# Kernel optimization log

Hardware: AMD Instinct MI355X
Metric: run time of the kernel (lower is better)

The kernel has to match this reference:

```python
import jax, jax.numpy as jnp
import numpy as np

MAX_NORM = 1.0 - 1e-5


def _norm(x):
    return jnp.sqrt(jnp.sum(x * x, axis=-1, keepdims=True) + 1e-15)


def project(x):
    n = _norm(x)
    return jnp.where(n > MAX_NORM, x * (MAX_NORM / n), x)


def artanh(x):
    return jnp.arctanh(jnp.clip(x, -1.0 + 1e-7, 1.0 - 1e-7))


def expmap0(u):
    n = _norm(u)
    return project(jnp.tanh(n) * u / n)


def logmap0(x):
    x = project(x)
    n = _norm(x)
    return artanh(n) * x / n


def mobius_add(x, y):
    x2 = jnp.sum(x * x, -1, keepdims=True)
    y2 = jnp.sum(y * y, -1, keepdims=True)
    xy = jnp.sum(x * y, -1, keepdims=True)
    num = (1.0 + 2.0 * xy + y2) * x + (1.0 - x2) * y
    den = 1.0 + 2.0 * xy + x2 * y2
    return project(num / den)


def mobius_matvec(M, x):
    # M: [d, d]; x: [..., d]  ->  expmap0(M @ logmap0(x))
    return expmap0(jnp.einsum('...d,ed->...e', logmap0(x), M))


def mobius_pw(w, x):
    # pointwise (diagonal) mobius scaling
    return expmap0(w * logmap0(x))


def hyper_gru(seq, Wz, Wr, Wh, Uz, Ur, Uh, bz, br, bh):
    # seq: [S, B, H, d] -> outputs [S, B, H, d]; state is H points per sample in a d-dim Poincare ball
    def cell(h, x):
        z = jax.nn.sigmoid(logmap0(mobius_add(mobius_add(mobius_matvec(Wz, h), mobius_matvec(Uz, x)), bz)))
        r = jax.nn.sigmoid(logmap0(mobius_add(mobius_add(mobius_matvec(Wr, h), mobius_matvec(Ur, x)), br)))
        h_tilde = mobius_add(mobius_add(mobius_matvec(Wh, mobius_pw(r, h)), mobius_matvec(Uh, x)), bh)
        h_new = mobius_add(h, mobius_pw(z, mobius_add(-h, h_tilde)))
        return h_new, h_new
    h0 = jnp.zeros_like(seq[0])
    _, outs = jax.lax.scan(cell, h0, seq)
    return outs


def poinc_dist_sum(enc, lab):
    # enc: [B,S,H,d] (in-ball), lab: [L,H,d] (in-ball) -> sum_H poinc_dist : [B,S,L]
    e2 = jnp.sum(enc * enc, -1)                      # [B,S,H]
    l2 = jnp.sum(lab * lab, -1)                      # [L,H]
    el = jnp.einsum('bshd,lhd->bslh', enc, lab)      # [B,S,L,H] (avoids [B,S,L,H,d] diff)
    d2 = e2[:, :, None, :] + l2[None, None, :, :] - 2.0 * el
    denom = (1.0 - e2)[:, :, None, :] * (1.0 - l2)[None, None, :, :]
    z = 1.0 + 2.0 * d2 / jnp.maximum(denom, 1e-15)
    dist = jnp.arccosh(jnp.maximum(z, 1.0 + 1e-7))
    return jnp.sum(dist, axis=-1)                    # [B,S,L]


def _forward(x, word_embed, label_embed, Wz, Wr, Wh, Uz, Ur, Uh, bz, br, bh, W1, b1, W2, b2):
    we = project(word_embed)[x]                      # [B,S,H,d]
    seq = jnp.transpose(we, (1, 0, 2, 3))            # [S,B,H,d]
    outs = hyper_gru(seq, Wz, Wr, Wh, Uz, Ur, Uh, bz, br, bh)
    enc = jnp.transpose(outs, (0, 1, 2, 3))
    enc = jnp.transpose(outs, (1, 0, 2, 3))          # [B,S,H,d]
    inter = poinc_dist_sum(enc, project(label_embed))  # [B,S,L]
    inter = jnp.transpose(inter, (0, 2, 1))          # [B,L,S]
    h = jax.nn.relu(inter @ W1.T + b1)               # [B,L,S//2]
    out = (h @ W2.T + b2)[..., 0]                    # [B,L]
    return out


def setup_inputs() -> dict:
    key = jax.random.key(0)
    ks = jax.random.split(key, 16)
    B, S, L, H, D, V = 4, 512, 512, 32, 8, 30000
    sc = 1.0 / np.sqrt(D)
    x = jax.random.randint(ks[0], (B, S), 0, V)
    inp = {
        'x': x,
        'word_embed': 0.05 * jax.random.normal(ks[1], (V, H, D), jnp.float32),
        'label_embed': 0.05 * jax.random.normal(ks[2], (L, H, D), jnp.float32),
        'Wz': sc * jax.random.normal(ks[3], (D, D), jnp.float32),
        'Wr': sc * jax.random.normal(ks[4], (D, D), jnp.float32),
        'Wh': sc * jax.random.normal(ks[5], (D, D), jnp.float32),
        'Uz': sc * jax.random.normal(ks[6], (D, D), jnp.float32),
        'Ur': sc * jax.random.normal(ks[7], (D, D), jnp.float32),
        'Uh': sc * jax.random.normal(ks[8], (D, D), jnp.float32),
        'bz': 0.01 * jax.random.normal(ks[9], (D,), jnp.float32),
        'br': 0.01 * jax.random.normal(ks[10], (D,), jnp.float32),
        'bh': 0.01 * jax.random.normal(ks[11], (D,), jnp.float32),
        'W1': jax.random.normal(ks[12], (S // 2, S), jnp.float32) / np.sqrt(S),
        'b1': jnp.zeros((S // 2,), jnp.float32),
        'W2': jax.random.normal(ks[13], (1, S // 2), jnp.float32) / np.sqrt(S // 2),
        'b2': jnp.zeros((1,), jnp.float32),
    }
    return inp


def reference(x, word_embed, label_embed, Wz, Wr, Wh, Uz, Ur, Uh, bz, br, bh, W1, b1, W2, b2):
    return _forward(x, word_embed, label_embed, Wz, Wr, Wh, Uz, Ur, Uh, bz, br, bh, W1, b1, W2, b2)
```

## Files before the change

kernel.cpp:

```cpp
#include <hip/hip_runtime.h>
#include <math.h>

#define DEV __device__ __forceinline__

static constexpr int BB = 4, SS = 512, LL = 512, HH = 32;
static constexpr float MAXN  = 1.0f - 1e-5f;
static constexpr float MAXN2 = MAXN * MAXN;

DEV float rcpf(float x) { return __builtin_amdgcn_rcpf(x); }
DEV float rsqf(float x) { return __builtin_amdgcn_rsqf(x); }

DEV float dot8(const float* a, const float* b) {
  float s0 = a[0]*b[0], s1 = a[1]*b[1], s2 = a[2]*b[2], s3 = a[3]*b[3];
  float s4 = a[4]*b[4], s5 = a[5]*b[5], s6 = a[6]*b[6], s7 = a[7]*b[7];
  return ((s0+s1)+(s2+s3)) + ((s4+s5)+(s6+s7));
}

DEV void load8(float* d, const float* p) {
  float4 a = *(const float4*)p;
  float4 b = *(const float4*)(p + 4);
  d[0]=a.x; d[1]=a.y; d[2]=a.z; d[3]=a.w;
  d[4]=b.x; d[5]=b.y; d[6]=b.z; d[7]=b.w;
}

DEV void store8(float* p, const float* d) {
  *(float4*)p       = make_float4(d[0], d[1], d[2], d[3]);
  *(float4*)(p + 4) = make_float4(d[4], d[5], d[6], d[7]);
}

DEV void project8(float* x) {
  float n2 = dot8(x, x) + 1e-15f;
  if (n2 > MAXN2) {
    float s = MAXN * rsqf(n2);
    #pragma unroll
    for (int i = 0; i < 8; ++i) x[i] *= s;
  }
}

DEV void logmap0_8(float* o, const float* x) {
  float t[8];
  #pragma unroll
  for (int i = 0; i < 8; ++i) t[i] = x[i];
  project8(t);
  float n2 = dot8(t, t) + 1e-15f;
  float rs = rsqf(n2);
  float n  = n2 * rs;
  float c  = fminf(n, 1.0f - 1e-7f);
  float at = 0.34657359f * (__log2f(1.0f + c) - __log2f(1.0f - c));
  float r  = at * rs;
  #pragma unroll
  for (int i = 0; i < 8; ++i) o[i] = t[i] * r;
}

DEV void expmap0_8(float* o, const float* u) {
  float n2 = dot8(u, u) + 1e-15f;
  float rs = rsqf(n2);
  float n  = n2 * rs;
  float e  = __expf(2.0f * n);
  float th = 1.0f - 2.0f * rcpf(e + 1.0f);
  float r  = th * rs;
  #pragma unroll
  for (int i = 0; i < 8; ++i) o[i] = u[i] * r;
  project8(o);
}

DEV void matvec8(float* o, const float* M, const float* u) {
  #pragma unroll
  for (int e = 0; e < 8; ++e) o[e] = dot8(M + 8*e, u);
}

template<int CTRL>
DEV float dppf(float x) {
  int xi = __float_as_int(x);
  return __int_as_float(__builtin_amdgcn_update_dpp(xi, xi, CTRL, 0xF, 0xF, true));
}

DEV float grp8sum(float x) {
  x += dppf<0xB1>(x);
  x += dppf<0x4E>(x);
  x += dppf<0x141>(x);
  return x;
}

DEV void red2(float& a, float& b) {
  float t0 = dppf<0xB1>(a),  t1 = dppf<0xB1>(b);  a += t0; b += t1;
  float t2 = dppf<0x4E>(a),  t3 = dppf<0x4E>(b);  a += t2; b += t3;
  float t4 = dppf<0x141>(a), t5 = dppf<0x141>(b); a += t4; b += t5;
}

DEV void red3(float& a, float& b, float& c) {
  float t0 = dppf<0xB1>(a),  t1 = dppf<0xB1>(b),  t2 = dppf<0xB1>(c);
  a += t0; b += t1; c += t2;
  float t3 = dppf<0x4E>(a),  t4 = dppf<0x4E>(b),  t5 = dppf<0x4E>(c);
  a += t3; b += t4; c += t5;
  float t6 = dppf<0x141>(a), t7 = dppf<0x141>(b), t8 = dppf<0x141>(c);
  a += t6; b += t7; c += t8;
}

DEV void red4(float& a, float& b, float& c, float& d) {
  float t0 = dppf<0xB1>(a),  t1 = dppf<0xB1>(b),  t2 = dppf<0xB1>(c),  t3 = dppf<0xB1>(d);
  a += t0; b += t1; c += t2; d += t3;
  float t4 = dppf<0x4E>(a),  t5 = dppf<0x4E>(b),  t6 = dppf<0x4E>(c),  t7 = dppf<0x4E>(d);
  a += t4; b += t5; c += t6; d += t7;
  float t8 = dppf<0x141>(a), t9 = dppf<0x141>(b), ta = dppf<0x141>(c), tb = dppf<0x141>(d);
  a += t8; b += t9; c += ta; d += tb;
}

#define MV8(w, u0,u1,u2,u3,u4,u5,u6,u7) \
  ((((w[0]*(u0)) + (w[1]*(u1))) + ((w[2]*(u2)) + (w[3]*(u3)))) + \
   (((w[4]*(u4)) + (w[5]*(u5))) + ((w[6]*(u6)) + (w[7]*(u7)))))

DEV float lgscale(float n2) {
  float n2p = n2 + 1e-15f;
  float rs  = rsqf(n2p);
  float n   = n2p * rs;
  float c   = fminf(n, 1.0f - 1e-7f);
  float at  = 0.34657359f * (__log2f(1.0f + c) - __log2f(1.0f - c));
  return at * rs;
}

DEV float sigm(float x) { return rcpf(1.0f + __expf(-x)); }

DEV void gate_coeffs(float n2v, float dvc, float dvb,
                     float c2, float b2, float cb,
                     float& P, float& Q, float& R, float& g2_2) {
  float n2p = n2v + 1e-15f;
  float rsv = rsqf(n2p);
  float nv  = n2p * rsv;
  float e   = __expf(2.0f * nv);
  float th  = 1.0f - 2.0f * rcpf(e + 1.0f);
  float a_scale = th * rsv;
  float a2  = th * th;
  if (a2 > MAXN2) { float s = MAXN * rsqf(a2); a_scale *= s; a2 = MAXN2; }
  float xy1 = a_scale * dvc;
  float cx1 = 1.0f + 2.0f*xy1 + c2;
  float cy1 = 1.0f - a2;
  float rd1 = rcpf(1.0f + 2.0f*xy1 + a2*c2);
  float num2 = (cx1*cx1)*a2 + 2.0f*(cx1*cy1)*xy1 + (cy1*cy1)*c2;
  float g1_2 = num2 * (rd1*rd1);
  float e1 = rd1;
  if (g1_2 > MAXN2) { e1 *= MAXN * rsqf(g1_2); g1_2 = MAXN2; }
  float ab  = a_scale * dvb;
  float xy2 = e1 * (cx1*ab + cy1*cb);
  float cx2 = 1.0f + 2.0f*xy2 + b2;
  float cy2 = 1.0f - g1_2;
  float rd2 = rcpf(1.0f + 2.0f*xy2 + g1_2*b2);
  float n2b = (cx2*cx2)*g1_2 + 2.0f*(cx2*cy2)*xy2 + (cy2*cy2)*b2;
  g2_2 = n2b * (rd2*rd2);
  float e2s = rd2;
  if (g2_2 > MAXN2) { e2s *= MAXN * rsqf(g2_2); g2_2 = MAXN2; }
  float t = e2s * cx2 * e1;
  P = t * cx1 * a_scale;
  Q = t * cy1;
  R = e2s * cy2;
}

__global__ void prep_kernel(const int* __restrict__ x, const float* __restrict__ wemb,
                            const float* __restrict__ Uz, const float* __restrict__ Ur,
                            const float* __restrict__ Uh,
                            const float* __restrict__ bzp, const float* __restrict__ brp,
                            const float* __restrict__ bhp,
                            float* __restrict__ axz, float* __restrict__ axr, float* __restrict__ axh,
                            float* __restrict__ scB)
{
  int t = blockIdx.x * 256 + threadIdx.x;
  if (t >= BB * SS * HH) return;
  int hh = t & (HH - 1);
  int bs = t >> 5;
  int idx = x[bs];
  float we[8]; load8(we, wemb + ((size_t)idx * HH + hh) * 8);
  project8(we);
  float lx[8]; logmap0_8(lx, we);
  float bz[8], br[8], bh[8];
  load8(bz, bzp); load8(br, brp); load8(bh, bhp);
  float v[8], az[8], ar[8], ah[8];
  matvec8(v, Uz, lx); expmap0_8(az, v); store8(axz + (size_t)t * 8, az);
  matvec8(v, Ur, lx); expmap0_8(ar, v); store8(axr + (size_t)t * 8, ar);
  matvec8(v, Uh, lx); expmap0_8(ah, v); store8(axh + (size_t)t * 8, ah);
  float cz2 = dot8(az, az), cr2 = dot8(ar, ar), ch2 = dot8(ah, ah);
  float czb = dot8(az, bz), crb = dot8(ar, br), chb = dot8(ah, bh);
  *(float4*)(scB + (size_t)t * 8)     = make_float4(cz2, cr2, ch2, czb);
  *(float4*)(scB + (size_t)t * 8 + 4) = make_float4(crb, chb, 0.0f, 0.0f);
}

__global__ void label_kernel(const float* __restrict__ lemb,
                             float* __restrict__ labP, float* __restrict__ l2o)
{
  int t = blockIdx.x * 256 + threadIdx.x;
  if (t >= LL * HH) return;
  float lv[8]; load8(lv, lemb + (size_t)t * 8);
  project8(lv);
  store8(labP + (size_t)t * 8, lv);
  l2o[t] = dot8(lv, lv);
}

__global__ __launch_bounds__(64, 1) void gru_kernel(
    const float* __restrict__ Wzp, const float* __restrict__ Wrp, const float* __restrict__ Whp,
    const float* __restrict__ bzp, const float* __restrict__ brp, const float* __restrict__ bhp,
    const float* __restrict__ axz, const float* __restrict__ axr, const float* __restrict__ axh,
    const float* __restrict__ scB,
    float* __restrict__ enc, float* __restrict__ e2out)
{
  const int lane = threadIdx.x;
  const int d    = lane & 7;
  const bool hif = (lane & 8) != 0;
  const int cg   = lane >> 4;
  const int chain = blockIdx.x * 4 + cg;
  const int b = chain >> 5;
  const int h = chain & 31;

  const float* Wg     = hif ? Wrp : Wzp;
  const float* cgbase = hif ? axr : axz;

  float wg[8], wh[8];
  #pragma unroll
  for (int k = 0; k < 8; ++k) {
    wg[k] = Wg[d*8 + (d^k)];
    wh[k] = Whp[d*8 + (d^k)];
  }
  float bgv = (hif ? brp : bzp)[d];
  float bhv = bhp[d];
  float bg2 = grp8sum(bgv*bgv);
  float bh2 = grp8sum(bhv*bhv);

  float hv = 0.0f, h2 = 0.0f;

  size_t voff = ((size_t)b * SS * HH + h) * 8 + d;
  size_t soff = (size_t)b * SS * HH + h;

  float cgv = cgbase[voff];
  float chv = axh[voff];
  float4 sA = *(const float4*)(scB + soff * 8);
  float4 sB = *(const float4*)(scB + soff * 8 + 4);

  #pragma unroll 1
  for (int s = 0; s < SS; ++s) {
    size_t nvoff = voff + HH*8, nsoff = soff + HH;
    size_t pv = (s + 1 < SS) ? nvoff : voff;
    size_t ps = (s + 1 < SS) ? nsoff : soff;
    float ncg = cgbase[pv];
    float nch = axh[pv];
    float4 nsA = *(const float4*)(scB + ps * 8);
    float4 nsB = *(const float4*)(scB + ps * 8 + 4);

    float c2g  = hif ? sA.y : sA.x;
    float cbg  = hif ? sB.x : sA.w;
    float ch2v = sA.z;
    float chbv = sB.y;

    float dhch = hv * chv, dhbh = hv * bhv;
    red2(dhch, dhbh);

    float lsc = lgscale(h2);
    float lh  = hv * lsc;

    float l1 = dppf<0xB1>(lh), l2 = dppf<0x4E>(lh), l3 = dppf<0x1B>(lh), l7 = dppf<0x141>(lh);
    float l4 = dppf<0x1B>(l7), l5 = dppf<0x4E>(l7), l6 = dppf<0xB1>(l7);
    float vg = MV8(wg, lh, l1, l2, l3, l4, l5, l6, l7);

    float n2g = vg*vg, dgc = vg*cgv, dgb = vg*bgv;
    red3(n2g, dgc, dgb);

    float P, Q, R, g22;
    gate_coeffs(n2g, dgc, dgb, c2g, bg2, cbg, P, Q, R, g22);
    float g2  = P*vg + Q*cgv + R*bgv;
    float gsv = sigm(lgscale(g22) * g2);
    float gsw = dppf<0x128>(gsv);
    float rv  = hif ? gsv : gsw;
    float zv  = hif ? gsw : gsv;

    float u = rv * lh;
    float u1 = dppf<0xB1>(u), u2p = dppf<0x4E>(u), u3 = dppf<0x1B>(u), u7 = dppf<0x141>(u);
    float u4 = dppf<0x1B>(u7), u5 = dppf<0x4E>(u7), u6 = dppf<0xB1>(u7);
    float vh = MV8(wh, u, u1, u2p, u3, u4, u5, u6, u7);

    float n2h = vh*vh, rhc = vh*chv, rhb = vh*bhv, dhv = hv*vh;
    red4(n2h, rhc, rhb, dhv);

    float Ph, Qh, Rh, t42;
    gate_coeffs(n2h, rhc, rhb, ch2v, bh2, chbv, Ph, Qh, Rh, t42);
    float t4   = Ph*vh + Qh*chv + Rh*bhv;
    float dht4 = Ph*dhv + Qh*dhch + Rh*dhbh;

    float xym = -dht4;
    float cxm = 1.0f + 2.0f*xym + t42;
    float cym = 1.0f - h2;
    float rdm = rcpf(1.0f + 2.0f*xym + h2*t42);
    float m2  = ((cxm*cxm)*h2 + 2.0f*(cxm*cym)*xym + (cym*cym)*t42) * (rdm*rdm);
    float em  = rdm;
    if (m2 > MAXN2) { em *= MAXN * rsqf(m2); m2 = MAXN2; }
    float md = em * (cym*t4 - cxm*hv);

    float lmm = lgscale(m2);
    float w   = zv * (lmm * md);

    float n2w = w*w, dhw = hv*w;
    red2(n2w, dhw);

    float n2wp = n2w + 1e-15f;
    float rsw = rsqf(n2wp);
    float nw  = n2wp * rsw;
    float ew  = __expf(2.0f * nw);
    float thw = 1.0f - 2.0f * rcpf(ew + 1.0f);
    float esc = thw * rsw;
    float ee2 = thw * thw;
    if (ee2 > MAXN2) { esc *= MAXN * rsqf(ee2); ee2 = MAXN2; }

    float xyf = esc * dhw;
    float cxf = 1.0f + 2.0f*xyf + ee2;
    float cyf = 1.0f - h2;
    float rdf = rcpf(1.0f + 2.0f*xyf + h2*ee2);
    float hn2 = ((cxf*cxf)*h2 + 2.0f*(cxf*cyf)*xyf + (cyf*cyf)*ee2) * (rdf*rdf);
    float ef  = rdf;
    if (hn2 > MAXN2) { ef *= MAXN * rsqf(hn2); hn2 = MAXN2; }
    float hn = (ef*cxf)*hv + (ef*cyf*esc)*w;

    if (!hif) enc[voff] = hn;
    if ((lane & 15) == 0) e2out[soff] = hn2;

    hv = hn; h2 = hn2;
    cgv = ncg; chv = nch; sA = nsA; sB = nsB;
    voff = nvoff; soff = nsoff;
  }
}

DEV float pdist(float ee, float ll, float el) {
  float d2  = ee + ll - 2.0f * el;
  float den = fmaxf((1.0f - ee) * (1.0f - ll), 1e-15f);
  float z   = 1.0f + 2.0f * d2 * rcpf(den);
  z = fmaxf(z, 1.0f + 1e-7f);
  return 0.69314718f * __log2f(z + sqrtf(z*z - 1.0f));
}

__global__ __launch_bounds__(256) void dist_kernel(
    const float* __restrict__ enc, const float* __restrict__ e2,
    const float* __restrict__ labP, const float* __restrict__ l2,
    float* __restrict__ inter)
{
  int blk = blockIdx.x;
  int lt = blk & 15, st = (blk >> 4) & 15, b = blk >> 8;
  int li = threadIdx.x & 15, si = threadIdx.x >> 4;
  int s = st * 32 + si * 2, l = lt * 32 + li * 2;

  const float* er0 = enc + ((size_t)b * SS + s) * HH * 8;
  const float* er1 = er0 + HH * 8;
  const float* e20 = e2 + ((size_t)b * SS + s) * HH;
  const float* e21 = e20 + HH;
  const float* lr0 = labP + (size_t)l * HH * 8;
  const float* lr1 = lr0 + HH * 8;
  const float* l20 = l2 + (size_t)l * HH;
  const float* l21 = l20 + HH;

  float a00 = 0.f, a01 = 0.f, a10 = 0.f, a11 = 0.f;
  #pragma unroll 2
  for (int hh = 0; hh < HH; ++hh) {
    float ev0[8], ev1[8], lv0[8], lv1[8];
    load8(ev0, er0 + hh * 8); load8(ev1, er1 + hh * 8);
    load8(lv0, lr0 + hh * 8); load8(lv1, lr1 + hh * 8);
    float x00 = dot8(ev0, lv0), x01 = dot8(ev0, lv1);
    float x10 = dot8(ev1, lv0), x11 = dot8(ev1, lv1);
    float e0v = e20[hh], e1v = e21[hh], l0v = l20[hh], l1v = l21[hh];
    a00 += pdist(e0v, l0v, x00);
    a01 += pdist(e0v, l1v, x01);
    a10 += pdist(e1v, l0v, x10);
    a11 += pdist(e1v, l1v, x11);
  }
  float* o0 = inter + ((size_t)b * LL + l) * SS + s;
  o0[0] = a00; o0[1] = a10;
  o0[SS] = a01; o0[SS + 1] = a11;
}

__global__ __launch_bounds__(256) void mlp1_kernel(
    const float* __restrict__ inter, const float* __restrict__ W1,
    const float* __restrict__ b1, float* __restrict__ hbuf)
{
  __shared__ float As[32][33];
  __shared__ float Bs[32][33];
  int t = threadIdx.x;
  int nt = blockIdx.x & 7, mt = blockIdx.x >> 3;
  int row0 = mt * 32, j0 = nt * 32;
  int li = t >> 4, ji = t & 15;
  float acc00 = 0.f, acc01 = 0.f, acc10 = 0.f, acc11 = 0.f;

  for (int k0 = 0; k0 < 512; k0 += 32) {
    __syncthreads();
    {
      int l = t >> 3, kk = (t & 7) * 4;
      float4 v = *(const float4*)(inter + (size_t)(row0 + l) * 512 + k0 + kk);
      As[l][kk] = v.x; As[l][kk+1] = v.y; As[l][kk+2] = v.z; As[l][kk+3] = v.w;
      float4 w = *(const float4*)(W1 + (size_t)(j0 + l) * 512 + k0 + kk);
      Bs[kk][l] = w.x; Bs[kk+1][l] = w.y; Bs[kk+2][l] = w.z; Bs[kk+3][l] = w.w;
    }
    __syncthreads();
    #pragma unroll
    for (int kk = 0; kk < 32; ++kk) {
      float a0 = As[li][kk],  a1 = As[li + 16][kk];
      float b0 = Bs[kk][ji],  b1v = Bs[kk][ji + 16];
      acc00 = fmaf(a0, b0, acc00);
      acc01 = fmaf(a0, b1v, acc01);
      acc10 = fmaf(a1, b0, acc10);
      acc11 = fmaf(a1, b1v, acc11);
    }
  }
  float bj0 = b1[j0 + ji], bj1 = b1[j0 + ji + 16];
  hbuf[(size_t)(row0 + li)      * 256 + j0 + ji]      = fmaxf(acc00 + bj0, 0.f);
  hbuf[(size_t)(row0 + li)      * 256 + j0 + ji + 16] = fmaxf(acc01 + bj1, 0.f);
  hbuf[(size_t)(row0 + li + 16) * 256 + j0 + ji]      = fmaxf(acc10 + bj0, 0.f);
  hbuf[(size_t)(row0 + li + 16) * 256 + j0 + ji + 16] = fmaxf(acc11 + bj1, 0.f);
}

__global__ void mlp2_kernel(const float* __restrict__ hbuf, const float* __restrict__ W2,
                            const float* __restrict__ b2, float* __restrict__ out)
{
  int t = threadIdx.x;
  int row = blockIdx.x * 4 + (t >> 6);
  int lane = t & 63;
  float v = 0.f;
  #pragma unroll
  for (int p = 0; p < 4; ++p) {
    int j = lane + p * 64;
    v = fmaf(hbuf[(size_t)row * 256 + j], W2[j], v);
  }
  #pragma unroll
  for (int off = 32; off > 0; off >>= 1) v += __shfl_xor(v, off);
  if (lane == 0) out[row] = v + b2[0];
}

extern "C" void kernel_launch(void* const* d_in, const int* in_sizes, int n_in,
                              void* d_out, int out_size, void* d_ws, size_t ws_size,
                              hipStream_t stream) {
  (void)in_sizes; (void)n_in; (void)out_size; (void)ws_size;
  const int*   x    = (const int*)d_in[0];
  const float* wemb = (const float*)d_in[1];
  const float* lemb = (const float*)d_in[2];
  const float* Wz = (const float*)d_in[3];
  const float* Wr = (const float*)d_in[4];
  const float* Wh = (const float*)d_in[5];
  const float* Uz = (const float*)d_in[6];
  const float* Ur = (const float*)d_in[7];
  const float* Uh = (const float*)d_in[8];
  const float* bz = (const float*)d_in[9];
  const float* br = (const float*)d_in[10];
  const float* bh = (const float*)d_in[11];
  const float* W1 = (const float*)d_in[12];
  const float* b1 = (const float*)d_in[13];
  const float* W2 = (const float*)d_in[14];
  const float* b2 = (const float*)d_in[15];
  float* out = (float*)d_out;

  float* p = (float*)d_ws;
  const size_t NBSH  = (size_t)BB * SS * HH;
  const size_t NBSH8 = NBSH * 8;
  float* axz  = p; p += NBSH8;
  float* axr  = p; p += NBSH8;
  float* axh  = p; p += NBSH8;
  float* scB  = p; p += NBSH8;
  float* enc  = p; p += NBSH8;
  float* e2   = p; p += NBSH;
  float* labP = p; p += (size_t)LL * HH * 8;
  float* l2   = p; p += (size_t)LL * HH;
  float* inter= p; p += (size_t)BB * LL * SS;
  float* hbuf = p; p += (size_t)BB * LL * 256;

  prep_kernel <<<(BB * SS * HH) / 256, 256, 0, stream>>>(x, wemb, Uz, Ur, Uh, bz, br, bh,
                                                         axz, axr, axh, scB);
  label_kernel<<<(LL * HH) / 256, 256, 0, stream>>>(lemb, labP, l2);
  gru_kernel  <<<32, 64, 0, stream>>>(Wz, Wr, Wh, bz, br, bh,
                                      axz, axr, axh, scB, enc, e2);
  dist_kernel <<<BB * (SS / 32) * (LL / 32), 256, 0, stream>>>(enc, e2, labP, l2, inter);
  mlp1_kernel <<<512, 256, 0, stream>>>(inter, W1, b1, hbuf);
  mlp2_kernel <<<512, 256, 0, stream>>>(hbuf, W2, b2, out);
}
```

Before: 583.2 us.

## Interleave four GRU chains per wavefront and shorten the serial dependency chain

The GRU kernel now runs four independent recurrent chains per wavefront in an unrolled inner loop, using 8 blocks instead of 32. The aim is to hide the latency of the serial per-step dependency chain through instruction-level parallelism. It also applies the Wz/Wr matvec to the raw hidden state and scales by the logmap factor afterwards, so that reduction overlaps with lgscale and merges into one five-value DPP reduction. Projection clamps become branch-free selects and the artanh clamp is dropped. The trade-offs are the loss of inter-block parallelism on the device, higher register pressure, a small numerical change from the removed clamp, and stores now issued by every lane, including duplicate writes to enc and e2out.

```diff
diff --git a/kernel.cpp b/kernel.cpp
--- a/kernel.cpp
+++ b/kernel.cpp
@@ -88,15 +88,6 @@
   float t4 = dppf<0x141>(a), t5 = dppf<0x141>(b); a += t4; b += t5;
 }
 
-DEV void red3(float& a, float& b, float& c) {
-  float t0 = dppf<0xB1>(a),  t1 = dppf<0xB1>(b),  t2 = dppf<0xB1>(c);
-  a += t0; b += t1; c += t2;
-  float t3 = dppf<0x4E>(a),  t4 = dppf<0x4E>(b),  t5 = dppf<0x4E>(c);
-  a += t3; b += t4; c += t5;
-  float t6 = dppf<0x141>(a), t7 = dppf<0x141>(b), t8 = dppf<0x141>(c);
-  a += t6; b += t7; c += t8;
-}
-
 DEV void red4(float& a, float& b, float& c, float& d) {
   float t0 = dppf<0xB1>(a),  t1 = dppf<0xB1>(b),  t2 = dppf<0xB1>(c),  t3 = dppf<0xB1>(d);
   a += t0; b += t1; c += t2; d += t3;
@@ -106,6 +97,15 @@
   a += t8; b += t9; c += ta; d += tb;
 }
 
+DEV void red5(float& a, float& b, float& c, float& d, float& e) {
+  float t0 = dppf<0xB1>(a),  t1 = dppf<0xB1>(b),  t2 = dppf<0xB1>(c),  t3 = dppf<0xB1>(d),  t4 = dppf<0xB1>(e);
+  a += t0; b += t1; c += t2; d += t3; e += t4;
+  float u0 = dppf<0x4E>(a),  u1 = dppf<0x4E>(b),  u2 = dppf<0x4E>(c),  u3 = dppf<0x4E>(d),  u4 = dppf<0x4E>(e);
+  a += u0; b += u1; c += u2; d += u3; e += u4;
+  float v0 = dppf<0x141>(a), v1 = dppf<0x141>(b), v2 = dppf<0x141>(c), v3 = dppf<0x141>(d), v4 = dppf<0x141>(e);
+  a += v0; b += v1; c += v2; d += v3; e += v4;
+}
+
 #define MV8(w, u0,u1,u2,u3,u4,u5,u6,u7) \
   ((((w[0]*(u0)) + (w[1]*(u1))) + ((w[2]*(u2)) + (w[3]*(u3)))) + \
    (((w[4]*(u4)) + (w[5]*(u5))) + ((w[6]*(u6)) + (w[7]*(u7)))))
@@ -114,12 +114,18 @@
   float n2p = n2 + 1e-15f;
   float rs  = rsqf(n2p);
   float n   = n2p * rs;
-  float c   = fminf(n, 1.0f - 1e-7f);
-  float at  = 0.34657359f * (__log2f(1.0f + c) - __log2f(1.0f - c));
+  float at  = 0.34657359f * (__log2f(1.0f + n) - __log2f(1.0f - n));
   return at * rs;
 }
 
 DEV float sigm(float x) { return rcpf(1.0f + __expf(-x)); }
+
+DEV void clampP(float& scale, float& n2) {
+  float s = MAXN * rsqf(n2);
+  bool c = n2 > MAXN2;
+  scale = c ? scale * s : scale;
+  n2    = c ? MAXN2 : n2;
+}
 
 DEV void gate_coeffs(float n2v, float dvc, float dvb,
                      float c2, float b2, float cb,
@@ -131,24 +137,22 @@
   float th  = 1.0f - 2.0f * rcpf(e + 1.0f);
   float a_scale = th * rsv;
   float a2  = th * th;
-  if (a2 > MAXN2) { float s = MAXN * rsqf(a2); a_scale *= s; a2 = MAXN2; }
+  clampP(a_scale, a2);
   float xy1 = a_scale * dvc;
   float cx1 = 1.0f + 2.0f*xy1 + c2;
   float cy1 = 1.0f - a2;
   float rd1 = rcpf(1.0f + 2.0f*xy1 + a2*c2);
-  float num2 = (cx1*cx1)*a2 + 2.0f*(cx1*cy1)*xy1 + (cy1*cy1)*c2;
-  float g1_2 = num2 * (rd1*rd1);
+  float g1_2 = ((cx1*cx1)*a2 + 2.0f*(cx1*cy1)*xy1 + (cy1*cy1)*c2) * (rd1*rd1);
   float e1 = rd1;
-  if (g1_2 > MAXN2) { e1 *= MAXN * rsqf(g1_2); g1_2 = MAXN2; }
+  clampP(e1, g1_2);
   float ab  = a_scale * dvb;
   float xy2 = e1 * (cx1*ab + cy1*cb);
   float cx2 = 1.0f + 2.0f*xy2 + b2;
   float cy2 = 1.0f - g1_2;
   float rd2 = rcpf(1.0f + 2.0f*xy2 + g1_2*b2);
-  float n2b = (cx2*cx2)*g1_2 + 2.0f*(cx2*cy2)*xy2 + (cy2*cy2)*b2;
-  g2_2 = n2b * (rd2*rd2);
+  g2_2 = ((cx2*cx2)*g1_2 + 2.0f*(cx2*cy2)*xy2 + (cy2*cy2)*b2) * (rd2*rd2);
   float e2s = rd2;
-  if (g2_2 > MAXN2) { e2s *= MAXN * rsqf(g2_2); g2_2 = MAXN2; }
+  clampP(e2s, g2_2);
   float t = e2s * cx2 * e1;
   P = t * cx1 * a_scale;
   Q = t * cy1;
@@ -201,13 +205,11 @@
     const float* __restrict__ scB,
     float* __restrict__ enc, float* __restrict__ e2out)
 {
+  constexpr int ILP = 4;
   const int lane = threadIdx.x;
   const int d    = lane & 7;
   const bool hif = (lane & 8) != 0;
   const int cg   = lane >> 4;
-  const int chain = blockIdx.x * 4 + cg;
-  const int b = chain >> 5;
-  const int h = chain & 31;
 
   const float* Wg     = hif ? Wrp : Wzp;
   const float* cgbase = hif ? axr : axz;
@@ -223,104 +225,114 @@
   float bg2 = grp8sum(bgv*bgv);
   float bh2 = grp8sum(bhv*bhv);
 
-  float hv = 0.0f, h2 = 0.0f;
-
-  size_t voff = ((size_t)b * SS * HH + h) * 8 + d;
-  size_t soff = (size_t)b * SS * HH + h;
-
-  float cgv = cgbase[voff];
-  float chv = axh[voff];
-  float4 sA = *(const float4*)(scB + soff * 8);
-  float4 sB = *(const float4*)(scB + soff * 8 + 4);
+  float  hv[ILP], h2[ILP], cgv[ILP], chv[ILP];
+  float4 sA[ILP], sB[ILP];
+  int    voff[ILP], soff[ILP];
+
+  #pragma unroll
+  for (int j = 0; j < ILP; ++j) {
+    int chain = blockIdx.x * (4*ILP) + j*4 + cg;
+    int b = chain >> 5, h = chain & 31;
+    hv[j] = 0.0f; h2[j] = 0.0f;
+    voff[j] = (b * SS * HH + h) * 8 + d;
+    soff[j] = b * SS * HH + h;
+    cgv[j] = cgbase[voff[j]];
+    chv[j] = axh[voff[j]];
+    sA[j]  = *(const float4*)(scB + (size_t)soff[j] * 8);
+    sB[j]  = *(const float4*)(scB + (size_t)soff[j] * 8 + 4);
+  }
 
   #pragma unroll 1
   for (int s = 0; s < SS; ++s) {
-    size_t nvoff = voff + HH*8, nsoff = soff + HH;
-    size_t pv = (s + 1 < SS) ? nvoff : voff;
-    size_t ps = (s + 1 < SS) ? nsoff : soff;
-    float ncg = cgbase[pv];
-    float nch = axh[pv];
-    float4 nsA = *(const float4*)(scB + ps * 8);
-    float4 nsB = *(const float4*)(scB + ps * 8 + 4);
-
-    float c2g  = hif ? sA.y : sA.x;
-    float cbg  = hif ? sB.x : sA.w;
-    float ch2v = sA.z;
-    float chbv = sB.y;
-
-    float dhch = hv * chv, dhbh = hv * bhv;
-    red2(dhch, dhbh);
-
-    float lsc = lgscale(h2);
-    float lh  = hv * lsc;
-
-    float l1 = dppf<0xB1>(lh), l2 = dppf<0x4E>(lh), l3 = dppf<0x1B>(lh), l7 = dppf<0x141>(lh);
-    float l4 = dppf<0x1B>(l7), l5 = dppf<0x4E>(l7), l6 = dppf<0xB1>(l7);
-    float vg = MV8(wg, lh, l1, l2, l3, l4, l5, l6, l7);
-
-    float n2g = vg*vg, dgc = vg*cgv, dgb = vg*bgv;
-    red3(n2g, dgc, dgb);
-
-    float P, Q, R, g22;
-    gate_coeffs(n2g, dgc, dgb, c2g, bg2, cbg, P, Q, R, g22);
-    float g2  = P*vg + Q*cgv + R*bgv;
-    float gsv = sigm(lgscale(g22) * g2);
-    float gsw = dppf<0x128>(gsv);
-    float rv  = hif ? gsv : gsw;
-    float zv  = hif ? gsw : gsv;
-
-    float u = rv * lh;
-    float u1 = dppf<0xB1>(u), u2p = dppf<0x4E>(u), u3 = dppf<0x1B>(u), u7 = dppf<0x141>(u);
-    float u4 = dppf<0x1B>(u7), u5 = dppf<0x4E>(u7), u6 = dppf<0xB1>(u7);
-    float vh = MV8(wh, u, u1, u2p, u3, u4, u5, u6, u7);
-
-    float n2h = vh*vh, rhc = vh*chv, rhb = vh*bhv, dhv = hv*vh;
-    red4(n2h, rhc, rhb, dhv);
-
-    float Ph, Qh, Rh, t42;
-    gate_coeffs(n2h, rhc, rhb, ch2v, bh2, chbv, Ph, Qh, Rh, t42);
-    float t4   = Ph*vh + Qh*chv + Rh*bhv;
-    float dht4 = Ph*dhv + Qh*dhch + Rh*dhbh;
-
-    float xym = -dht4;
-    float cxm = 1.0f + 2.0f*xym + t42;
-    float cym = 1.0f - h2;
-    float rdm = rcpf(1.0f + 2.0f*xym + h2*t42);
-    float m2  = ((cxm*cxm)*h2 + 2.0f*(cxm*cym)*xym + (cym*cym)*t42) * (rdm*rdm);
-    float em  = rdm;
-    if (m2 > MAXN2) { em *= MAXN * rsqf(m2); m2 = MAXN2; }
-    float md = em * (cym*t4 - cxm*hv);
-
-    float lmm = lgscale(m2);
-    float w   = zv * (lmm * md);
-
-    float n2w = w*w, dhw = hv*w;
-    red2(n2w, dhw);
-
-    float n2wp = n2w + 1e-15f;
-    float rsw = rsqf(n2wp);
-    float nw  = n2wp * rsw;
-    float ew  = __expf(2.0f * nw);
-    float thw = 1.0f - 2.0f * rcpf(ew + 1.0f);
-    float esc = thw * rsw;
-    float ee2 = thw * thw;
-    if (ee2 > MAXN2) { esc *= MAXN * rsqf(ee2); ee2 = MAXN2; }
-
-    float xyf = esc * dhw;
-    float cxf = 1.0f + 2.0f*xyf + ee2;
-    float cyf = 1.0f - h2;
-    float rdf = rcpf(1.0f + 2.0f*xyf + h2*ee2);
-    float hn2 = ((cxf*cxf)*h2 + 2.0f*(cxf*cyf)*xyf + (cyf*cyf)*ee2) * (rdf*rdf);
-    float ef  = rdf;
-    if (hn2 > MAXN2) { ef *= MAXN * rsqf(hn2); hn2 = MAXN2; }
-    float hn = (ef*cxf)*hv + (ef*cyf*esc)*w;
-
-    if (!hif) enc[voff] = hn;
-    if ((lane & 15) == 0) e2out[soff] = hn2;
-
-    hv = hn; h2 = hn2;
-    cgv = ncg; chv = nch; sA = nsA; sB = nsB;
-    voff = nvoff; soff = nsoff;
+    #pragma unroll
+    for (int j = 0; j < ILP; ++j) {
+      int nvo = voff[j] + HH*8, nso = soff[j] + HH;
+      float  ncg = cgbase[nvo];
+      float  nch = axh[nvo];
+      float4 nsA = *(const float4*)(scB + (size_t)nso * 8);
+      float4 nsB = *(const float4*)(scB + (size_t)nso * 8 + 4);
+
+      float c2g  = hif ? sA[j].y : sA[j].x;
+      float cbg  = hif ? sB[j].x : sA[j].w;
+      float ch2v = sA[j].z;
+      float chbv = sB[j].y;
+
+      float hvj = hv[j], h2j = h2[j];
+      float p1 = dppf<0xB1>(hvj), p2 = dppf<0x4E>(hvj), p3 = dppf<0x1B>(hvj), p7 = dppf<0x141>(hvj);
+      float p4 = dppf<0x1B>(p7),  p5 = dppf<0x4E>(p7),  p6 = dppf<0xB1>(p7);
+      float vg0 = MV8(wg, hvj, p1, p2, p3, p4, p5, p6, p7);
+
+      float n2g0 = vg0*vg0, dgc0 = vg0*cgv[j], dgb0 = vg0*bgv;
+      float dhch = hvj*chv[j], dhbh = hvj*bhv;
+      red5(n2g0, dgc0, dgb0, dhch, dhbh);
+
+      float lsc = lgscale(h2j);
+      float lh  = hvj * lsc;
+      float vg  = vg0 * lsc;
+      float l2s = lsc * lsc;
+      float n2g = n2g0 * l2s, dgc = dgc0 * lsc, dgb = dgb0 * lsc;
+
+      float P, Q, R, g22;
+      gate_coeffs(n2g, dgc, dgb, c2g, bg2, cbg, P, Q, R, g22);
+      float g2  = P*vg + Q*cgv[j] + R*bgv;
+      float gsv = sigm(lgscale(g22) * g2);
+      float gsw = dppf<0x128>(gsv);
+      float rv  = hif ? gsv : gsw;
+      float zv  = hif ? gsw : gsv;
+
+      float u  = rv * lh;
+      float q1 = dppf<0xB1>(u), q2 = dppf<0x4E>(u), q3 = dppf<0x1B>(u), q7 = dppf<0x141>(u);
+      float q4 = dppf<0x1B>(q7), q5 = dppf<0x4E>(q7), q6 = dppf<0xB1>(q7);
+      float vh = MV8(wh, u, q1, q2, q3, q4, q5, q6, q7);
+
+      float n2h = vh*vh, rhc = vh*chv[j], rhb = vh*bhv, dhv = hvj*vh;
+      red4(n2h, rhc, rhb, dhv);
+
+      float Ph, Qh, Rh, t42;
+      gate_coeffs(n2h, rhc, rhb, ch2v, bh2, chbv, Ph, Qh, Rh, t42);
+      float t4   = Ph*vh + Qh*chv[j] + Rh*bhv;
+      float dht4 = Ph*dhv + Qh*dhch + Rh*dhbh;
+
+      float xym = -dht4;
+      float cxm = 1.0f + 2.0f*xym + t42;
+      float cym = 1.0f - h2j;
+      float rdm = rcpf(1.0f + 2.0f*xym + h2j*t42);
+      float m2  = ((cxm*cxm)*h2j + 2.0f*(cxm*cym)*xym + (cym*cym)*t42) * (rdm*rdm);
+      float em  = rdm;
+      clampP(em, m2);
+      float md = em * (cym*t4 - cxm*hvj);
+
+      float lmm = lgscale(m2);
+      float w   = zv * (lmm * md);
+
+      float n2w = w*w, dhw = hvj*w;
+      red2(n2w, dhw);
+
+      float n2wp = n2w + 1e-15f;
+      float rsw = rsqf(n2wp);
+      float nw  = n2wp * rsw;
+      float ew  = __expf(2.0f * nw);
+      float thw = 1.0f - 2.0f * rcpf(ew + 1.0f);
+      float esc = thw * rsw;
+      float ee2 = thw * thw;
+      clampP(esc, ee2);
+
+      float xyf = esc * dhw;
+      float cxf = 1.0f + 2.0f*xyf + ee2;
+      float cyf = 1.0f - h2j;
+      float rdf = rcpf(1.0f + 2.0f*xyf + h2j*ee2);
+      float hn2 = ((cxf*cxf)*h2j + 2.0f*(cxf*cyf)*xyf + (cyf*cyf)*ee2) * (rdf*rdf);
+      float ef  = rdf;
+      clampP(ef, hn2);
+      float hn = (ef*cxf)*hvj + (ef*cyf*esc)*w;
+
+      enc[voff[j]]   = hn;
+      e2out[soff[j]] = hn2;
+
+      hv[j] = hn; h2[j] = hn2;
+      cgv[j] = ncg; chv[j] = nch; sA[j] = nsA; sB[j] = nsB;
+      voff[j] = nvo; soff[j] = nso;
+    }
   }
 }
 
@@ -465,8 +477,8 @@
   prep_kernel <<<(BB * SS * HH) / 256, 256, 0, stream>>>(x, wemb, Uz, Ur, Uh, bz, br, bh,
                                                          axz, axr, axh, scB);
   label_kernel<<<(LL * HH) / 256, 256, 0, stream>>>(lemb, labP, l2);
-  gru_kernel  <<<32, 64, 0, stream>>>(Wz, Wr, Wh, bz, br, bh,
-                                      axz, axr, axh, scB, enc, e2);
+  gru_kernel  <<<8, 64, 0, stream>>>(Wz, Wr, Wh, bz, br, bh,
+                                     axz, axr, axh, scB, enc, e2);
   dist_kernel <<<BB * (SS / 32) * (LL / 32), 256, 0, stream>>>(enc, e2, labP, l2, inter);
   mlp1_kernel <<<512, 256, 0, stream>>>(inter, W1, b1, hbuf);
   mlp2_kernel <<<512, 256, 0, stream>>>(hbuf, W2, b2, out);
```

Result: slower. 2.102 ms (+260.4%).
